# Kernel tuning notes

Hardware: AMD Instinct MI355X
Metric: run time of the kernel (lower is better)

Reference implementation:

```python
import jax, jax.numpy as jnp
import numpy as np

NA, NB, MAXNB = 100000, 200000, 6
ATOM_FDIM, BOND_FDIM, H, DEPTH = 133, 147, 300, 3


def setup_inputs() -> dict:
    key = jax.random.key(0)
    ks = jax.random.split(key, 8)
    # index 0 is the zero-padding entry (chemprop convention)
    f_atoms = jax.random.normal(ks[0], (NA, ATOM_FDIM), jnp.float32).at[0].set(0.0)
    f_bonds = jax.random.normal(ks[1], (NB, BOND_FDIM), jnp.float32).at[0].set(0.0)
    a2b = jax.random.randint(ks[2], (NA, MAXNB), 0, NB)
    b2a = jax.random.randint(ks[3], (NB,), 0, NA)
    b2revb = jax.random.randint(ks[4], (NB,), 0, NB)
    W_i = jax.random.normal(ks[5], (BOND_FDIM, H), jnp.float32) * (1.0 / np.sqrt(BOND_FDIM))
    W_h = jax.random.normal(ks[6], (H, H), jnp.float32) * (1.0 / np.sqrt(H))
    W_o = jax.random.normal(ks[7], (ATOM_FDIM + H, H), jnp.float32) * (1.0 / np.sqrt(ATOM_FDIM + H))
    b_o = jnp.zeros((H,), jnp.float32)
    return {"f_atoms": f_atoms, "f_bonds": f_bonds, "a2b": a2b, "b2a": b2a,
            "b2revb": b2revb, "W_i": W_i, "W_h": W_h, "W_o": W_o, "b_o": b_o}


def reference(f_atoms, f_bonds, a2b, b2a, b2revb, W_i, W_h, W_o, b_o):
    # bond-message D-MPNN forward (atom_messages=False, attention=False,
    # undirected=False, dropout=0 / eval mode)
    inp = f_bonds @ W_i                     # [NB, H]
    message = jax.nn.relu(inp)              # [NB, H]
    for _ in range(DEPTH - 1):
        # gather incoming bond messages per atom and sum over neighbors
        a_message = message[a2b].sum(axis=1)          # [NA, MAXNB, H] -> [NA, H]
        message = a_message[b2a] - message[b2revb]    # [NB, H]
        message = jax.nn.relu(inp + message @ W_h)
    a_message = message[a2b].sum(axis=1)              # [NA, H]
    a_input = jnp.concatenate([f_atoms, a_message], axis=1)  # [NA, ATOM_FDIM+H]
    atom_hiddens = jax.nn.relu(a_input @ W_o + b_o)   # [NA, H]
    # the per-molecule narrow loop in the original merely re-slices
    # atom_hiddens by a_scope; the concatenation of all slices == atom_hiddens
    return atom_hiddens
```

## Files before the change

### kernel.cpp

```cpp
#include <hip/hip_runtime.h>
#include <hip/hip_fp16.h>

#define NA 100000
#define NB 200000
#define MAXNB 6
#define AF 133
#define BF 147
#define H 300
#define HP 320
#define AFP 160
#define NP 320
#define KP_C 480
#define BM 128
#define BN 320
#define BK 32
#define NTH 512
#define LDK 40

typedef _Float16 f16;
typedef __attribute__((ext_vector_type(8))) _Float16 f16x8;
typedef __attribute__((ext_vector_type(4))) float f32x4;

__global__ void conv_pad_f16(const float* __restrict__ src, f16* __restrict__ dst,
                             int M, int Ks) {
  int idx = blockIdx.x * blockDim.x + threadIdx.x;
  if (idx >= M * (AFP / 8)) return;
  int r = idx / (AFP / 8);
  int c = (idx - r * (AFP / 8)) * 8;
  f16x8 o;
#pragma unroll
  for (int j = 0; j < 8; ++j) {
    int k = c + j;
    o[j] = (k < Ks) ? (f16)src[(size_t)r * Ks + k] : (f16)0.0f;
  }
  *(f16x8*)&dst[(size_t)r * AFP + c] = o;
}

__global__ void prep_w1(const float* __restrict__ Wi, const float* __restrict__ Wh,
                        f16* __restrict__ dst) {
  int idx = blockIdx.x * blockDim.x + threadIdx.x;
  if (idx >= NP * KP_C) return;
  int n = idx / KP_C, k = idx - n * KP_C;
  float v = 0.0f;
  if (n < H) {
    if (k < BF) v = Wi[(size_t)k * H + n];
    else if (k >= AFP && k < AFP + H) v = Wh[(size_t)(k - AFP) * H + n];
  }
  dst[idx] = (f16)v;
}

__global__ void prep_wo(const float* __restrict__ src, f16* __restrict__ dst) {
  int idx = blockIdx.x * blockDim.x + threadIdx.x;
  if (idx >= NP * KP_C) return;
  int n = idx / KP_C, k = idx - n * KP_C;
  int ks = -1;
  if (k < AF) ks = k;
  else if (k >= AFP && k < AFP + H) ks = AF + (k - AFP);
  float v = (n < H && ks >= 0) ? src[(size_t)ks * H + n] : 0.0f;
  dst[idx] = (f16)v;
}

__global__ void gather_sum_kernel(const f16* __restrict__ msg,
                                  const int* __restrict__ a2b,
                                  f16* __restrict__ amsg) {
  int idx = blockIdx.x * blockDim.x + threadIdx.x;
  if (idx >= NA * (HP / 8)) return;
  int a = idx / (HP / 8);
  int c = (idx - a * (HP / 8)) * 8;
  const int* nbr = &a2b[(size_t)a * MAXNB];
  float acc[8] = {0.f, 0.f, 0.f, 0.f, 0.f, 0.f, 0.f, 0.f};
#pragma unroll
  for (int t = 0; t < MAXNB; ++t) {
    int r = nbr[t];
    f16x8 v = *(const f16x8*)&msg[(size_t)r * HP + c];
#pragma unroll
    for (int j = 0; j < 8; ++j) acc[j] += (float)v[j];
  }
  f16x8 o;
#pragma unroll
  for (int j = 0; j < 8; ++j) o[j] = (f16)acc[j];
  *(f16x8*)&amsg[(size_t)a * HP + c] = o;
}

template <int MODE>
__global__ __launch_bounds__(NTH)
void gemm_kernel(const f16* __restrict__ Afp,
                 const f16* __restrict__ amsg,
                 const f16* __restrict__ msg_in,
                 const int* __restrict__ b2a,
                 const int* __restrict__ b2revb,
                 const int* __restrict__ a2b,
                 const f16* __restrict__ Wp,
                 const float* __restrict__ b_o,
                 f16* __restrict__ out_msg,
                 float* __restrict__ out_f32) {
  constexpr int KSTEPS = (MODE == 0) ? 5 : 15;
  constexpr int ASTEPS = 5;
  constexpr int M = (MODE == 2) ? NA : NB;

  __shared__ f16 As[2][BM][LDK];
  __shared__ f16 Bs[2][BN][LDK];

  const int mb = blockIdx.x;
  const int tid = threadIdx.x;
  const int lane = tid & 63, wid = tid >> 6;
  const int wr = wid >> 2, wc = wid & 3;

  f32x4 acc[4][5] = {};

  const int arow = tid >> 2;
  const int ac = (tid & 3) * 8;
  const int m_g = mb * BM + arow;
  const int mrow = (m_g < M) ? m_g : 0;

  const int bidx2 = tid + 2 * NTH;
  const int br0 = tid >> 2,            bc0 = (tid & 3) * 8;
  const int br1 = (tid + NTH) >> 2,    bc1 = ((tid + NTH) & 3) * 8;
  const int br2 = bidx2 >> 2,          bc2 = (bidx2 & 3) * 8;
  const bool b2ok = bidx2 < BN * 4;

  int ra = 0, rb = 0;
  int n0 = 0, n1 = 0, n2 = 0, n3 = 0, n4 = 0, n5 = 0;
  if constexpr (MODE == 1) { ra = b2a[mrow]; rb = b2revb[mrow]; }
  if constexpr (MODE == 2) {
    const int* p = &a2b[(size_t)mrow * MAXNB];
    n0 = p[0]; n1 = p[1]; n2 = p[2]; n3 = p[3]; n4 = p[4]; n5 = p[5];
  }

  f16x8 ax, ay, av0, av1, av2, av3, av4, av5, pw0, pw1, pw2;

  auto issue_loads = [&](int ks) {
    const int kb = ks * BK + ac;
    if constexpr (MODE == 0) {
      ax = *(const f16x8*)&Afp[(size_t)mrow * AFP + kb];
    } else if constexpr (MODE == 1) {
      if (ks < ASTEPS) {
        ax = *(const f16x8*)&Afp[(size_t)mrow * AFP + kb];
      } else {
        const int kk = kb - AFP;
        ax = *(const f16x8*)&amsg[(size_t)ra * HP + kk];
        ay = *(const f16x8*)&msg_in[(size_t)rb * HP + kk];
      }
    } else {
      if (ks < ASTEPS) {
        ax = *(const f16x8*)&Afp[(size_t)mrow * AFP + kb];
      } else {
        const int kk = kb - AFP;
        av0 = *(const f16x8*)&msg_in[(size_t)n0 * HP + kk];
        av1 = *(const f16x8*)&msg_in[(size_t)n1 * HP + kk];
        av2 = *(const f16x8*)&msg_in[(size_t)n2 * HP + kk];
        av3 = *(const f16x8*)&msg_in[(size_t)n3 * HP + kk];
        av4 = *(const f16x8*)&msg_in[(size_t)n4 * HP + kk];
        av5 = *(const f16x8*)&msg_in[(size_t)n5 * HP + kk];
      }
    }
    const int kw = ks * BK;
    pw0 = *(const f16x8*)&Wp[(size_t)br0 * KP_C + kw + bc0];
    pw1 = *(const f16x8*)&Wp[(size_t)br1 * KP_C + kw + bc1];
    if (b2ok) pw2 = *(const f16x8*)&Wp[(size_t)br2 * KP_C + kw + bc2];
  };

  auto write_lds = [&](int buf, int ks) {
    f16x8 pa = ax;
    if constexpr (MODE == 1) {
      if (ks >= ASTEPS) pa = ax - ay;
    }
    if constexpr (MODE == 2) {
      if (ks >= ASTEPS) pa = ((av0 + av1) + (av2 + av3)) + (av4 + av5);
    }
    *(f16x8*)&As[buf][arow][ac] = pa;
    *(f16x8*)&Bs[buf][br0][bc0] = pw0;
    *(f16x8*)&Bs[buf][br1][bc1] = pw1;
    if (b2ok) *(f16x8*)&Bs[buf][br2][bc2] = pw2;
  };

  issue_loads(0);
  write_lds(0, 0);
  issue_loads(1);
  __syncthreads();

  const int row16 = lane & 15, kh = (lane >> 4) * 8;

  for (int ks = 0; ks < KSTEPS; ++ks) {
    const int cur = ks & 1;
    f16x8 af[4], bfr[5];
#pragma unroll
    for (int m = 0; m < 4; ++m)
      af[m] = *(const f16x8*)&As[cur][wr * 64 + m * 16 + row16][kh];
#pragma unroll
    for (int n = 0; n < 5; ++n)
      bfr[n] = *(const f16x8*)&Bs[cur][wc * 80 + n * 16 + row16][kh];
#pragma unroll
    for (int m = 0; m < 4; ++m)
#pragma unroll
      for (int n = 0; n < 5; ++n)
        acc[m][n] = __builtin_amdgcn_mfma_f32_16x16x32_f16(af[m], bfr[n], acc[m][n], 0, 0, 0);

    if (ks + 1 < KSTEPS) write_lds(cur ^ 1, ks + 1);
    if (ks + 2 < KSTEPS) issue_loads(ks + 2);
    __syncthreads();
  }

  const int rquad = (lane >> 4) * 4;
#pragma unroll
  for (int m = 0; m < 4; ++m) {
#pragma unroll
    for (int n = 0; n < 5; ++n) {
      const int col = wc * 80 + n * 16 + row16;
#pragma unroll
      for (int j = 0; j < 4; ++j) {
        const int row = mb * BM + wr * 64 + m * 16 + rquad + j;
        float v = acc[m][n][j];
        if constexpr (MODE == 2) {
          if (row < M && col < H)
            out_f32[(size_t)row * H + col] = fmaxf(v + b_o[col], 0.0f);
        } else {
          if (row < M)
            out_msg[(size_t)row * HP + col] = (f16)fmaxf(v, 0.0f);
        }
      }
    }
  }
}

extern "C" void kernel_launch(void* const* d_in, const int* in_sizes, int n_in,
                              void* d_out, int out_size, void* d_ws, size_t ws_size,
                              hipStream_t stream) {
  const float* f_atoms = (const float*)d_in[0];
  const float* f_bonds = (const float*)d_in[1];
  const int*   a2b     = (const int*)d_in[2];
  const int*   b2a     = (const int*)d_in[3];
  const int*   b2revb  = (const int*)d_in[4];
  const float* W_i     = (const float*)d_in[5];
  const float* W_h     = (const float*)d_in[6];
  const float* W_o     = (const float*)d_in[7];
  const float* b_o     = (const float*)d_in[8];
  float* out = (float*)d_out;

  char* ws = (char*)d_ws;
  size_t off = 0;
  f16* msgA = (f16*)(ws + off); off += (size_t)NB * HP * 2;
  f16* msgB = (f16*)(ws + off); off += (size_t)NB * HP * 2;
  f16* amsg = (f16*)(ws + off); off += (size_t)NA * HP * 2;
  f16* fb16 = (f16*)(ws + off); off += (size_t)NB * AFP * 2;
  f16* fa16 = (f16*)(ws + off); off += (size_t)NA * AFP * 2;
  f16* W1P  = (f16*)(ws + off); off += (size_t)NP * KP_C * 2;
  f16* WoP  = (f16*)(ws + off); off += (size_t)NP * KP_C * 2;
  if (off > ws_size) return;

  prep_w1<<<(NP * KP_C + 255) / 256, 256, 0, stream>>>(W_i, W_h, W1P);
  prep_wo<<<(NP * KP_C + 255) / 256, 256, 0, stream>>>(W_o, WoP);
  conv_pad_f16<<<(NB * (AFP / 8) + 255) / 256, 256, 0, stream>>>(f_bonds, fb16, NB, BF);
  conv_pad_f16<<<(NA * (AFP / 8) + 255) / 256, 256, 0, stream>>>(f_atoms, fa16, NA, AF);

  const int gB = (NB + BM - 1) / BM;
  const int gA = (NA + BM - 1) / BM;
  dim3 gS((NA * (HP / 8) + 255) / 256);

  gemm_kernel<0><<<gB, NTH, 0, stream>>>(fb16, nullptr, nullptr,
                                         nullptr, nullptr, nullptr, W1P, nullptr,
                                         msgA, nullptr);
  gather_sum_kernel<<<gS, 256, 0, stream>>>(msgA, a2b, amsg);
  gemm_kernel<1><<<gB, NTH, 0, stream>>>(fb16, amsg, msgA,
                                         b2a, b2revb, nullptr, W1P, nullptr,
                                         msgB, nullptr);
  gather_sum_kernel<<<gS, 256, 0, stream>>>(msgB, a2b, amsg);
  gemm_kernel<1><<<gB, NTH, 0, stream>>>(fb16, amsg, msgB,
                                         b2a, b2revb, nullptr, W1P, nullptr,
                                         msgA, nullptr);
  gemm_kernel<2><<<gA, NTH, 0, stream>>>(fa16, nullptr, msgA,
                                         nullptr, nullptr, a2b, WoP, b_o,
                                         nullptr, out);
}
```

Measured before the change: 712.4 us.

## Deepen A-operand prefetch pipeline with double register sets and 2x unrolled loop

```diff
diff --git a/kernel.cpp b/kernel.cpp
--- a/kernel.cpp
+++ b/kernel.cpp
@@ -97,6 +97,7 @@
   constexpr int KSTEPS = (MODE == 0) ? 5 : 15;
   constexpr int ASTEPS = 5;
   constexpr int M = (MODE == 2) ? NA : NB;
+  constexpr bool DEEP = (MODE != 2);
 
   __shared__ f16 As[2][BM][LDK];
   __shared__ f16 Bs[2][BN][LDK];
@@ -127,9 +128,11 @@
     n0 = p[0]; n1 = p[1]; n2 = p[2]; n3 = p[3]; n4 = p[4]; n5 = p[5];
   }
 
-  f16x8 ax, ay, av0, av1, av2, av3, av4, av5, pw0, pw1, pw2;
-
-  auto issue_loads = [&](int ks) {
+  f16x8 axA, ayA, avA[6];
+  f16x8 axB, ayB, avB[6];
+  f16x8 pw0, pw1, pw2;
+
+  auto issueA = [&](int ks, f16x8& ax, f16x8& ay, f16x8 (&av)[6]) {
     const int kb = ks * BK + ac;
     if constexpr (MODE == 0) {
       ax = *(const f16x8*)&Afp[(size_t)mrow * AFP + kb];
@@ -146,27 +149,30 @@
         ax = *(const f16x8*)&Afp[(size_t)mrow * AFP + kb];
       } else {
         const int kk = kb - AFP;
-        av0 = *(const f16x8*)&msg_in[(size_t)n0 * HP + kk];
-        av1 = *(const f16x8*)&msg_in[(size_t)n1 * HP + kk];
-        av2 = *(const f16x8*)&msg_in[(size_t)n2 * HP + kk];
-        av3 = *(const f16x8*)&msg_in[(size_t)n3 * HP + kk];
-        av4 = *(const f16x8*)&msg_in[(size_t)n4 * HP + kk];
-        av5 = *(const f16x8*)&msg_in[(size_t)n5 * HP + kk];
+        av[0] = *(const f16x8*)&msg_in[(size_t)n0 * HP + kk];
+        av[1] = *(const f16x8*)&msg_in[(size_t)n1 * HP + kk];
+        av[2] = *(const f16x8*)&msg_in[(size_t)n2 * HP + kk];
+        av[3] = *(const f16x8*)&msg_in[(size_t)n3 * HP + kk];
+        av[4] = *(const f16x8*)&msg_in[(size_t)n4 * HP + kk];
+        av[5] = *(const f16x8*)&msg_in[(size_t)n5 * HP + kk];
       }
     }
+  };
+
+  auto issueB = [&](int ks) {
     const int kw = ks * BK;
     pw0 = *(const f16x8*)&Wp[(size_t)br0 * KP_C + kw + bc0];
     pw1 = *(const f16x8*)&Wp[(size_t)br1 * KP_C + kw + bc1];
     if (b2ok) pw2 = *(const f16x8*)&Wp[(size_t)br2 * KP_C + kw + bc2];
   };
 
-  auto write_lds = [&](int buf, int ks) {
+  auto write_lds = [&](int buf, int ks, f16x8& ax, f16x8& ay, f16x8 (&av)[6]) {
     f16x8 pa = ax;
     if constexpr (MODE == 1) {
       if (ks >= ASTEPS) pa = ax - ay;
     }
     if constexpr (MODE == 2) {
-      if (ks >= ASTEPS) pa = ((av0 + av1) + (av2 + av3)) + (av4 + av5);
+      if (ks >= ASTEPS) pa = ((av[0] + av[1]) + (av[2] + av[3])) + (av[4] + av[5]);
     }
     *(f16x8*)&As[buf][arow][ac] = pa;
     *(f16x8*)&Bs[buf][br0][bc0] = pw0;
@@ -174,31 +180,43 @@
     if (b2ok) *(f16x8*)&Bs[buf][br2][bc2] = pw2;
   };
 
-  issue_loads(0);
-  write_lds(0, 0);
-  issue_loads(1);
-  __syncthreads();
-
   const int row16 = lane & 15, kh = (lane >> 4) * 8;
 
-  for (int ks = 0; ks < KSTEPS; ++ks) {
-    const int cur = ks & 1;
+  auto compute = [&](int buf) {
     f16x8 af[4], bfr[5];
 #pragma unroll
     for (int m = 0; m < 4; ++m)
-      af[m] = *(const f16x8*)&As[cur][wr * 64 + m * 16 + row16][kh];
+      af[m] = *(const f16x8*)&As[buf][wr * 64 + m * 16 + row16][kh];
 #pragma unroll
     for (int n = 0; n < 5; ++n)
-      bfr[n] = *(const f16x8*)&Bs[cur][wc * 80 + n * 16 + row16][kh];
+      bfr[n] = *(const f16x8*)&Bs[buf][wc * 80 + n * 16 + row16][kh];
 #pragma unroll
     for (int m = 0; m < 4; ++m)
 #pragma unroll
       for (int n = 0; n < 5; ++n)
         acc[m][n] = __builtin_amdgcn_mfma_f32_16x16x32_f16(af[m], bfr[n], acc[m][n], 0, 0, 0);
-
-    if (ks + 1 < KSTEPS) write_lds(cur ^ 1, ks + 1);
-    if (ks + 2 < KSTEPS) issue_loads(ks + 2);
+  };
+
+  issueA(0, axA, ayA, avA); issueB(0);
+  write_lds(0, 0, axA, ayA, avA);
+  issueA(1, axB, ayB, avB); issueB(1);
+  __syncthreads();
+
+  for (int ks = 0; ks < KSTEPS; ks += 2) {
+    if (DEEP && ks + 2 < KSTEPS) issueA(ks + 2, axA, ayA, avA);
+    compute(0);
+    if (ks + 1 < KSTEPS) write_lds(1, ks + 1, axB, ayB, avB);
+    if (!DEEP && ks + 2 < KSTEPS) issueA(ks + 2, axA, ayA, avA);
+    if (ks + 2 < KSTEPS) issueB(ks + 2);
     __syncthreads();
+    if (ks + 1 < KSTEPS) {
+      if (DEEP && ks + 3 < KSTEPS) issueA(ks + 3, axB, ayB, avB);
+      compute(1);
+      if (ks + 2 < KSTEPS) write_lds(0, ks + 2, axA, ayA, avA);
+      if (!DEEP && ks + 3 < KSTEPS) issueA(ks + 3, axB, ayB, avB);
+      if (ks + 3 < KSTEPS) issueB(ks + 3);
+      __syncthreads();
+    }
   }
 
   const int rquad = (lane >> 4) * 4;
```

After: 692.8 us. 2.8% less time.
